# Kernel optimization log

Hardware: AMD Instinct MI355X
Metric: run time of the kernel (lower is better)

## Reference

```python
import jax, jax.numpy as jnp
import numpy as np

NUM_USERS = 100000
NUM_ITEMS = 50000
D = 64            # args.recdim
N_LAYERS = 3      # args.layer
NNZ = 4800000     # edges in the normalized bipartite adjacency (COO)
N = NUM_USERS + NUM_ITEMS


def setup_inputs() -> dict:
    key = jax.random.key(0)
    k1, k2, k3, k4, k5 = jax.random.split(key, 5)
    # LightGCN inits embeddings with normal(std=0.1)
    user_emb = 0.1 * jax.random.normal(k1, (NUM_USERS, D), dtype=jnp.float32)
    item_emb = 0.1 * jax.random.normal(k2, (NUM_ITEMS, D), dtype=jnp.float32)
    adj_rows = jax.random.randint(k3, (NNZ,), 0, N)
    adj_cols = jax.random.randint(k4, (NNZ,), 0, N)
    # stand-in for D^{-1/2} A D^{-1/2} normalized values
    adj_vals = jax.random.uniform(k5, (NNZ,), dtype=jnp.float32)
    return {"user_emb": user_emb, "item_emb": item_emb,
            "adj_vals": adj_vals, "adj_rows": adj_rows, "adj_cols": adj_cols}


def _spmm(rows, cols, vals, x, n):
    # sparse [n,n] @ dense [n,d] via gather + segment-sum (COO SpMM)
    return jax.ops.segment_sum(vals[:, None] * x[cols], rows, num_segments=n)


def reference(user_emb, item_emb, adj_vals, adj_rows, adj_cols):
    n_users = user_emb.shape[0]
    n = n_users + item_emb.shape[0]
    all_emb = jnp.concatenate([user_emb, item_emb], axis=0)  # [N, D]
    embs = [all_emb]
    for _ in range(N_LAYERS):  # fixed small hop count
        all_emb = _spmm(adj_rows, adj_cols, adj_vals, all_emb, n)
        embs.append(all_emb)
    light_out = jnp.mean(jnp.stack(embs, axis=1), axis=1)  # [N, D]
    users = light_out[:n_users]
    items = light_out[n_users:]
    return users, items
```

## Files before the change

kernel.cpp:

```cpp
#include <hip/hip_runtime.h>


#define NUSERS 100000
#define NITEMS 50000
#define NTOT   150000
#define DIM    64
#define NNZ_E  4800000

#define RPB     512
#define RSH     9
#define NBUCK   ((NTOT + RPB - 1) / RPB)
#define CHUNK_E 8192
#define NPART   ((NNZ_E + CHUNK_E - 1) / CHUNK_E)

__device__ __forceinline__ unsigned short benc(float f) {
    union { float f; unsigned u; } t; t.f = f;
    unsigned r = t.u + 0x7FFFu + ((t.u >> 16) & 1u);
    return (unsigned short)(r >> 16);
}
__device__ __forceinline__ float blo(unsigned g) { return __uint_as_float(g << 16); }
__device__ __forceinline__ float bhi(unsigned g) { return __uint_as_float(g & 0xFFFF0000u); }

__global__ void __launch_bounds__(512)
partA1_kernel(const int* __restrict__ rows, int* __restrict__ cntmatT) {
    __shared__ int l[NBUCK];
    int p = blockIdx.x;
    int c0 = p * CHUNK_E;
    int c1 = c0 + CHUNK_E; if (c1 > NNZ_E) c1 = NNZ_E;
    for (int k = threadIdx.x; k < NBUCK; k += 512) l[k] = 0;
    __syncthreads();
    for (int e = c0 + threadIdx.x; e < c1; e += 512)
        atomicAdd(&l[rows[e] >> RSH], 1);
    __syncthreads();
    for (int k = threadIdx.x; k < NBUCK; k += 512)
        cntmatT[(size_t)k * NPART + p] = l[k];
}

__global__ void __launch_bounds__(1024)
colscan1_kernel(const int* __restrict__ cntmatT, int* __restrict__ runoffT,
                int* __restrict__ colTotal) {
    __shared__ int t[1024];
    int b = blockIdx.x;
    int tid = threadIdx.x;
    int v = (tid < NPART) ? cntmatT[(size_t)b * NPART + tid] : 0;
    t[tid] = v;
    __syncthreads();
    for (int ofs = 1; ofs < 1024; ofs <<= 1) {
        int a = (tid >= ofs) ? t[tid - ofs] : 0;
        __syncthreads();
        t[tid] += a;
        __syncthreads();
    }
    if (tid < NPART) runoffT[(size_t)b * NPART + tid] = t[tid] - v;
    if (tid == NPART - 1) colTotal[b] = t[tid];
}

__global__ void colscan2_kernel(const int* __restrict__ colTotal, int* __restrict__ bptr) {
    __shared__ int t[512];
    int tid = threadIdx.x;
    int v = (tid < NBUCK) ? colTotal[tid] : 0;
    t[tid] = v;
    __syncthreads();
    for (int ofs = 1; ofs < 512; ofs <<= 1) {
        int a = (tid >= ofs) ? t[tid - ofs] : 0;
        __syncthreads();
        t[tid] += a;
        __syncthreads();
    }
    if (tid < NBUCK) bptr[tid] = t[tid] - v;
    if (tid == 511) bptr[NBUCK] = t[511];
}

__global__ void __launch_bounds__(512)
partA2_kernel(const int* __restrict__ rows, const int* __restrict__ cols,
              const float* __restrict__ vals, const int* __restrict__ runoffT,
              const int* __restrict__ bptr, int2* __restrict__ tmp) {
    __shared__ int cur[NBUCK];
    int p = blockIdx.x;
    int c0 = p * CHUNK_E;
    int c1 = c0 + CHUNK_E; if (c1 > NNZ_E) c1 = NNZ_E;
    for (int k = threadIdx.x; k < NBUCK; k += 512)
        cur[k] = bptr[k] + runoffT[(size_t)k * NPART + p];
    __syncthreads();
    for (int e = c0 + threadIdx.x; e < c1; e += 512) {
        int r = rows[e];
        int b = r >> RSH, rl = r & (RPB - 1);
        int q = atomicAdd(&cur[b], 1);
        tmp[q] = make_int2(cols[e] | (rl << 18), __float_as_int(vals[e]));
    }
}

__global__ void __launch_bounds__(1024)
partB_kernel(const int* __restrict__ bptr, const int2* __restrict__ tmp,
             unsigned* __restrict__ fin, int* __restrict__ rowptr) {
    __shared__ int cnt[RPB];
    __shared__ int cur[RPB];
    int b = blockIdx.x;
    int bb0 = bptr[b], bb1 = bptr[b + 1];
    int tid = threadIdx.x;
    if (tid < RPB) cnt[tid] = 0;
    __syncthreads();
    for (int e = bb0 + tid; e < bb1; e += 1024)
        atomicAdd(&cnt[((unsigned)tmp[e].x) >> 18], 1);
    __syncthreads();
    int v = 0;
    if (tid < RPB) { v = cnt[tid]; cur[tid] = v; }
    __syncthreads();
    for (int ofs = 1; ofs < RPB; ofs <<= 1) {
        int a = (tid < RPB && tid >= ofs) ? cur[tid - ofs] : 0;
        __syncthreads();
        if (tid < RPB) cur[tid] += a;
        __syncthreads();
    }
    if (tid < RPB) {
        int excl = cur[tid] - v;
        int row = b * RPB + tid;
        if (row < NTOT) rowptr[row] = bb0 + excl;
        cur[tid] = excl;
    }
    if (b == NBUCK - 1 && tid == 0) rowptr[NTOT] = bb1;
    __syncthreads();
    for (int e = bb0 + tid; e < bb1; e += 1024) {
        int2 t = tmp[e];
        int rl = ((unsigned)t.x) >> 18;
        int q = bb0 + atomicAdd(&cur[rl], 1);
        float val = __int_as_float(t.y);
        unsigned qq = (unsigned)__float2int_rn(val * 16384.f);
        if (qq > 16383u) qq = 16383u;
        fin[q] = (((unsigned)t.x & 0x3FFFFu) << 14) | qq;
    }
}

__global__ void convert_kernel(const float2* __restrict__ user, const float2* __restrict__ item,
                               unsigned* __restrict__ xh2) {
    int i = blockIdx.x * blockDim.x + threadIdx.x;
    if (i >= NTOT * 32) return;
    float2 v = (i < NUSERS * 32) ? user[i] : item[i - NUSERS * 32];
    xh2[i] = (unsigned)benc(v.x) | ((unsigned)benc(v.y) << 16);
}

__global__ void __launch_bounds__(256)
spmm_kernel(const int* __restrict__ rowptr, const unsigned* __restrict__ ed,
            const uint4* __restrict__ xin, uint4* __restrict__ yout,
            const float4* __restrict__ user, const float4* __restrict__ item,
            const uint4* __restrict__ y1, float4* __restrict__ out, int last) {
    int wid = blockIdx.x * (blockDim.x >> 6) + (threadIdx.x >> 6);
    int lane = threadIdx.x & 63;
    int oct = lane >> 3, s = lane & 7;
    int r = wid * 8 + oct;
    if (r >= NTOT) return;
    int start = rowptr[r];
    int end   = rowptr[r + 1];
    const float SCL = 1.f / 16384.f;
    float a0 = 0.f, a1 = 0.f, a2 = 0.f, a3 = 0.f, a4 = 0.f, a5 = 0.f, a6 = 0.f, a7 = 0.f;
    int i = start;
    for (; i + 8 <= end; i += 8) {
        unsigned e[8];
#pragma unroll
        for (int u = 0; u < 8; ++u) e[u] = ed[i + u];
        uint4 g[8];
#pragma unroll
        for (int u = 0; u < 8; ++u) g[u] = xin[(size_t)(e[u] >> 14) * 8 + s];
#pragma unroll
        for (int u = 0; u < 8; ++u) {
            float v = (float)(e[u] & 0x3FFFu) * SCL;
            a0 += v * blo(g[u].x); a1 += v * bhi(g[u].x);
            a2 += v * blo(g[u].y); a3 += v * bhi(g[u].y);
            a4 += v * blo(g[u].z); a5 += v * bhi(g[u].z);
            a6 += v * blo(g[u].w); a7 += v * bhi(g[u].w);
        }
    }
    for (; i < end; ++i) {
        unsigned e = ed[i];
        uint4 g = xin[(size_t)(e >> 14) * 8 + s];
        float v = (float)(e & 0x3FFFu) * SCL;
        a0 += v * blo(g.x); a1 += v * bhi(g.x);
        a2 += v * blo(g.y); a3 += v * bhi(g.y);
        a4 += v * blo(g.z); a5 += v * bhi(g.z);
        a6 += v * blo(g.w); a7 += v * bhi(g.w);
    }
    if (!last) {
        uint4 o;
        o.x = (unsigned)benc(a0) | ((unsigned)benc(a1) << 16);
        o.y = (unsigned)benc(a2) | ((unsigned)benc(a3) << 16);
        o.z = (unsigned)benc(a4) | ((unsigned)benc(a5) << 16);
        o.w = (unsigned)benc(a6) | ((unsigned)benc(a7) << 16);
        yout[(size_t)r * 8 + s] = o;
    } else {
        size_t f4 = (size_t)r * 16 + 2 * s;
        float4 x0a = (r < NUSERS) ? user[f4]     : item[f4     - (size_t)NUSERS * 16];
        float4 x0b = (r < NUSERS) ? user[f4 + 1] : item[f4 + 1 - (size_t)NUSERS * 16];
        uint4 u1 = y1[(size_t)r * 8 + s];
        uint4 u2 = xin[(size_t)r * 8 + s];
        float4 oa, ob;
        oa.x = 0.25f * (x0a.x + blo(u1.x) + blo(u2.x) + a0);
        oa.y = 0.25f * (x0a.y + bhi(u1.x) + bhi(u2.x) + a1);
        oa.z = 0.25f * (x0a.z + blo(u1.y) + blo(u2.y) + a2);
        oa.w = 0.25f * (x0a.w + bhi(u1.y) + bhi(u2.y) + a3);
        ob.x = 0.25f * (x0b.x + blo(u1.z) + blo(u2.z) + a4);
        ob.y = 0.25f * (x0b.y + bhi(u1.z) + bhi(u2.z) + a5);
        ob.z = 0.25f * (x0b.z + blo(u1.w) + blo(u2.w) + a6);
        ob.w = 0.25f * (x0b.w + bhi(u1.w) + bhi(u2.w) + a7);
        out[f4]     = oa;
        out[f4 + 1] = ob;
    }
}

extern "C" void kernel_launch(void* const* d_in, const int* in_sizes, int n_in,
                              void* d_out, int out_size, void* d_ws, size_t ws_size,
                              hipStream_t stream) {
    const float* user = (const float*)d_in[0];
    const float* item = (const float*)d_in[1];
    const float* vals = (const float*)d_in[2];
    const int*   rows = (const int*)d_in[3];
    const int*   cols = (const int*)d_in[4];
    float* out = (float*)d_out;

    char* w = (char*)d_ws;
    int2*     tmp      = (int2*)w;     w += (size_t)NNZ_E * 8;
    unsigned* fin      = (unsigned*)w; w += (size_t)NNZ_E * 4;
    unsigned* bufA     = (unsigned*)w; w += (size_t)NTOT * DIM * 2;
    unsigned* bufB     = (unsigned*)w; w += (size_t)NTOT * DIM * 2;
    int*      rowptr   = (int*)w;      w += (size_t)(NTOT + 1) * 4;
    int*      cntmatT  = (int*)w;      w += (size_t)NPART * NBUCK * 4;
    int*      runoffT  = (int*)w;      w += (size_t)NPART * NBUCK * 4;
    int*      colTotal = (int*)w;      w += (size_t)NBUCK * 4;
    int*      bptr     = (int*)w;

    const int blk = 256;
    const int gConv = (NTOT * 32 + blk - 1) / blk;
    const int gSpmm = (NTOT / 8 + 3) / 4;

    partA1_kernel<<<NPART, 512, 0, stream>>>(rows, cntmatT);
    colscan1_kernel<<<NBUCK, 1024, 0, stream>>>(cntmatT, runoffT, colTotal);
    colscan2_kernel<<<1, 512, 0, stream>>>(colTotal, bptr);
    partA2_kernel<<<NPART, 512, 0, stream>>>(rows, cols, vals, runoffT, bptr, tmp);
    partB_kernel<<<NBUCK, 1024, 0, stream>>>(bptr, tmp, fin, rowptr);

    convert_kernel<<<gConv, blk, 0, stream>>>((const float2*)user, (const float2*)item, bufA);

    spmm_kernel<<<gSpmm, blk, 0, stream>>>(rowptr, fin, (const uint4*)bufA, (uint4*)bufB,
                                           (const float4*)user, (const float4*)item,
                                           (const uint4*)bufB, (float4*)out, 0);
    spmm_kernel<<<gSpmm, blk, 0, stream>>>(rowptr, fin, (const uint4*)bufB, (uint4*)bufA,
                                           (const float4*)user, (const float4*)item,
                                           (const uint4*)bufB, (float4*)out, 0);
    spmm_kernel<<<gSpmm, blk, 0, stream>>>(rowptr, fin, (const uint4*)bufA, (uint4*)bufA,
                                           (const float4*)user, (const float4*)item,
                                           (const uint4*)bufB, (float4*)out, 1);
}
```

Baseline: 531.2 us.

## Fuse edge partition passes with local chunk sort and column-binned row ordering

Replaces the separate count and scatter passes with a single per-chunk kernel that sorts each chunk by bucket in shared memory and writes it contiguously. The second pass gathers each bucket's segments through a binary search over chunk offsets. Within each row it also orders edges by column block to improve locality of the SpMM gathers. Buckets shrink to 256 rows, and edge values are now quantized to 12 bits instead of 14 to make room for the column index. This trades accuracy and extra per-edge search work for fewer global scatter passes and better cache behavior in the three SpMM layers.

```diff
diff --git a/kernel.cpp b/kernel.cpp
--- a/kernel.cpp
+++ b/kernel.cpp
@@ -7,11 +7,14 @@
 #define DIM    64
 #define NNZ_E  4800000
 
-#define RPB     512
-#define RSH     9
-#define NBUCK   ((NTOT + RPB - 1) / RPB)
+#define RPB     256
+#define RSH     8
+#define NBUCK   586
 #define CHUNK_E 8192
 #define NPART   ((NNZ_E + CHUNK_E - 1) / CHUNK_E)
+#define NCB     37
+#define CSH     12
+#define NBIN    (RPB * NCB)
 
 __device__ __forceinline__ unsigned short benc(float f) {
     union { float f; unsigned u; } t; t.f = f;
@@ -22,27 +25,73 @@
 __device__ __forceinline__ float bhi(unsigned g) { return __uint_as_float(g & 0xFFFF0000u); }
 
 __global__ void __launch_bounds__(512)
-partA1_kernel(const int* __restrict__ rows, int* __restrict__ cntmatT) {
-    __shared__ int l[NBUCK];
+partA2_kernel(const int* __restrict__ rows, const int* __restrict__ cols,
+              const float* __restrict__ vals, int* __restrict__ cntmat,
+              int* __restrict__ segoff, int2* __restrict__ tmp) {
+    __shared__ int2 buf[CHUNK_E];
+    __shared__ int cnt[NBUCK];
+    __shared__ int st[512];
     int p = blockIdx.x;
     int c0 = p * CHUNK_E;
     int c1 = c0 + CHUNK_E; if (c1 > NNZ_E) c1 = NNZ_E;
-    for (int k = threadIdx.x; k < NBUCK; k += 512) l[k] = 0;
-    __syncthreads();
-    for (int e = c0 + threadIdx.x; e < c1; e += 512)
-        atomicAdd(&l[rows[e] >> RSH], 1);
-    __syncthreads();
-    for (int k = threadIdx.x; k < NBUCK; k += 512)
-        cntmatT[(size_t)k * NPART + p] = l[k];
+    int nb = c1 - c0;
+    int tid = threadIdx.x;
+    for (int k = tid; k < NBUCK; k += 512) cnt[k] = 0;
+    __syncthreads();
+    int rloc[16];
+#pragma unroll
+    for (int u = 0; u < 16; ++u) {
+        int e = c0 + tid + u * 512;
+        rloc[u] = (e < c1) ? rows[e] : -1;
+        if (rloc[u] >= 0) atomicAdd(&cnt[rloc[u] >> RSH], 1);
+    }
+    __syncthreads();
+    int t0 = tid * 2;
+    int cA = (t0     < NBUCK) ? cnt[t0]     : 0;
+    int cB = (t0 + 1 < NBUCK) ? cnt[t0 + 1] : 0;
+    int s = cA + cB;
+    st[tid] = s;
+    __syncthreads();
+    for (int ofs = 1; ofs < 512; ofs <<= 1) {
+        int a = (tid >= ofs) ? st[tid - ofs] : 0;
+        __syncthreads();
+        st[tid] += a;
+        __syncthreads();
+    }
+    int P = st[tid] - s;
+    if (t0 < NBUCK) {
+        cnt[t0] = P;
+        segoff[(size_t)p * NBUCK + t0] = P;
+        cntmat[(size_t)p * NBUCK + t0] = cA;
+    }
+    if (t0 + 1 < NBUCK) {
+        cnt[t0 + 1] = P + cA;
+        segoff[(size_t)p * NBUCK + t0 + 1] = P + cA;
+        cntmat[(size_t)p * NBUCK + t0 + 1] = cB;
+    }
+    __syncthreads();
+#pragma unroll
+    for (int u = 0; u < 16; ++u) {
+        int e = c0 + tid + u * 512;
+        if (rloc[u] >= 0) {
+            int r = rloc[u];
+            int b = r >> RSH, rl = r & (RPB - 1);
+            int q = atomicAdd(&cnt[b], 1);
+            buf[q] = make_int2(cols[e] | (rl << 18), __float_as_int(vals[e]));
+        }
+    }
+    __syncthreads();
+    for (int k = tid; k < nb; k += 512)
+        tmp[c0 + k] = buf[k];
 }
 
 __global__ void __launch_bounds__(1024)
-colscan1_kernel(const int* __restrict__ cntmatT, int* __restrict__ runoffT,
+colscan1_kernel(const int* __restrict__ cntmat, int* __restrict__ runoffT,
                 int* __restrict__ colTotal) {
     __shared__ int t[1024];
     int b = blockIdx.x;
     int tid = threadIdx.x;
-    int v = (tid < NPART) ? cntmatT[(size_t)b * NPART + tid] : 0;
+    int v = (tid < NPART) ? cntmat[(size_t)tid * NBUCK + b] : 0;
     t[tid] = v;
     __syncthreads();
     for (int ofs = 1; ofs < 1024; ofs <<= 1) {
@@ -51,83 +100,96 @@
         t[tid] += a;
         __syncthreads();
     }
-    if (tid < NPART) runoffT[(size_t)b * NPART + tid] = t[tid] - v;
-    if (tid == NPART - 1) colTotal[b] = t[tid];
-}
-
-__global__ void colscan2_kernel(const int* __restrict__ colTotal, int* __restrict__ bptr) {
-    __shared__ int t[512];
+    if (tid < NPART) runoffT[(size_t)b * (NPART + 1) + tid] = t[tid] - v;
+    if (tid == NPART - 1) {
+        runoffT[(size_t)b * (NPART + 1) + NPART] = t[tid];
+        colTotal[b] = t[tid];
+    }
+}
+
+__global__ void __launch_bounds__(1024)
+colscan2_kernel(const int* __restrict__ colTotal, int* __restrict__ bptr) {
+    __shared__ int t[1024];
     int tid = threadIdx.x;
     int v = (tid < NBUCK) ? colTotal[tid] : 0;
     t[tid] = v;
     __syncthreads();
-    for (int ofs = 1; ofs < 512; ofs <<= 1) {
+    for (int ofs = 1; ofs < 1024; ofs <<= 1) {
         int a = (tid >= ofs) ? t[tid - ofs] : 0;
         __syncthreads();
         t[tid] += a;
         __syncthreads();
     }
     if (tid < NBUCK) bptr[tid] = t[tid] - v;
-    if (tid == 511) bptr[NBUCK] = t[511];
-}
-
-__global__ void __launch_bounds__(512)
-partA2_kernel(const int* __restrict__ rows, const int* __restrict__ cols,
-              const float* __restrict__ vals, const int* __restrict__ runoffT,
-              const int* __restrict__ bptr, int2* __restrict__ tmp) {
-    __shared__ int cur[NBUCK];
-    int p = blockIdx.x;
-    int c0 = p * CHUNK_E;
-    int c1 = c0 + CHUNK_E; if (c1 > NNZ_E) c1 = NNZ_E;
-    for (int k = threadIdx.x; k < NBUCK; k += 512)
-        cur[k] = bptr[k] + runoffT[(size_t)k * NPART + p];
-    __syncthreads();
-    for (int e = c0 + threadIdx.x; e < c1; e += 512) {
-        int r = rows[e];
-        int b = r >> RSH, rl = r & (RPB - 1);
-        int q = atomicAdd(&cur[b], 1);
-        tmp[q] = make_int2(cols[e] | (rl << 18), __float_as_int(vals[e]));
-    }
+    if (tid == 1023) bptr[NBUCK] = t[1023];
 }
 
 __global__ void __launch_bounds__(1024)
-partB_kernel(const int* __restrict__ bptr, const int2* __restrict__ tmp,
-             unsigned* __restrict__ fin, int* __restrict__ rowptr) {
-    __shared__ int cnt[RPB];
-    __shared__ int cur[RPB];
+partBF_kernel(const int* __restrict__ bptr, const int* __restrict__ runoffT,
+              const int* __restrict__ segoff, const int2* __restrict__ tmp,
+              unsigned* __restrict__ fin, int* __restrict__ rowptr) {
+    __shared__ int cnt[NBIN];
+    __shared__ int st[1024];
+    __shared__ int runoff[NPART + 1];
+    __shared__ int soff[NPART];
     int b = blockIdx.x;
-    int bb0 = bptr[b], bb1 = bptr[b + 1];
+    int bb0 = bptr[b];
     int tid = threadIdx.x;
-    if (tid < RPB) cnt[tid] = 0;
-    __syncthreads();
-    for (int e = bb0 + tid; e < bb1; e += 1024)
-        atomicAdd(&cnt[((unsigned)tmp[e].x) >> 18], 1);
-    __syncthreads();
-    int v = 0;
-    if (tid < RPB) { v = cnt[tid]; cur[tid] = v; }
-    __syncthreads();
-    for (int ofs = 1; ofs < RPB; ofs <<= 1) {
-        int a = (tid < RPB && tid >= ofs) ? cur[tid - ofs] : 0;
-        __syncthreads();
-        if (tid < RPB) cur[tid] += a;
-        __syncthreads();
-    }
+    for (int k = tid; k < NBIN; k += 1024) cnt[k] = 0;
+    if (tid <= NPART) runoff[tid] = runoffT[(size_t)b * (NPART + 1) + tid];
+    if (tid < NPART)  soff[tid]   = segoff[(size_t)tid * NBUCK + b];
+    __syncthreads();
+    int nb = runoff[NPART];
+    for (int j = tid; j < nb; j += 1024) {
+        int lo = 0, hi = NPART;
+        while (hi - lo > 1) { int mid = (lo + hi) >> 1; if (runoff[mid] <= j) lo = mid; else hi = mid; }
+        int src = lo * CHUNK_E + soff[lo] + (j - runoff[lo]);
+        int x = tmp[src].x;
+        int key = ((x >> 18) & 255) * NCB + ((x & 0x3FFFF) >> CSH);
+        atomicAdd(&cnt[key], 1);
+    }
+    __syncthreads();
+    int t0 = tid * 10;
+    int c[10];
+    int s = 0;
+#pragma unroll
+    for (int u = 0; u < 10; ++u) {
+        int idx = t0 + u;
+        c[u] = (idx < NBIN) ? cnt[idx] : 0;
+        s += c[u];
+    }
+    st[tid] = s;
+    __syncthreads();
+    for (int ofs = 1; ofs < 1024; ofs <<= 1) {
+        int a = (tid >= ofs) ? st[tid - ofs] : 0;
+        __syncthreads();
+        st[tid] += a;
+        __syncthreads();
+    }
+    int P = st[tid] - s;
+#pragma unroll
+    for (int u = 0; u < 10; ++u) {
+        int idx = t0 + u;
+        if (idx < NBIN) { cnt[idx] = P; P += c[u]; }
+    }
+    __syncthreads();
     if (tid < RPB) {
-        int excl = cur[tid] - v;
-        int row = b * RPB + tid;
-        if (row < NTOT) rowptr[row] = bb0 + excl;
-        cur[tid] = excl;
-    }
-    if (b == NBUCK - 1 && tid == 0) rowptr[NTOT] = bb1;
-    __syncthreads();
-    for (int e = bb0 + tid; e < bb1; e += 1024) {
-        int2 t = tmp[e];
-        int rl = ((unsigned)t.x) >> 18;
-        int q = bb0 + atomicAdd(&cur[rl], 1);
-        float val = __int_as_float(t.y);
-        unsigned qq = (unsigned)__float2int_rn(val * 16384.f);
-        if (qq > 16383u) qq = 16383u;
-        fin[q] = (((unsigned)t.x & 0x3FFFFu) << 14) | qq;
+        int r = b * RPB + tid;
+        if (r < NTOT) rowptr[r] = bb0 + cnt[tid * NCB];
+    }
+    if (b == NBUCK - 1 && tid == 0) rowptr[NTOT] = bb0 + nb;
+    __syncthreads();
+    for (int j = tid; j < nb; j += 1024) {
+        int lo = 0, hi = NPART;
+        while (hi - lo > 1) { int mid = (lo + hi) >> 1; if (runoff[mid] <= j) lo = mid; else hi = mid; }
+        int src = lo * CHUNK_E + soff[lo] + (j - runoff[lo]);
+        int2 t = tmp[src];
+        int x = t.x;
+        int key = ((x >> 18) & 255) * NCB + ((x & 0x3FFFF) >> CSH);
+        int q = atomicAdd(&cnt[key], 1);
+        unsigned qq = (unsigned)__float2int_rn(__int_as_float(t.y) * 4096.f);
+        if (qq > 4095u) qq = 4095u;
+        fin[bb0 + q] = ((unsigned)x & 0x3FFFFu) | (qq << 20);
     }
 }
 
@@ -151,7 +213,7 @@
     if (r >= NTOT) return;
     int start = rowptr[r];
     int end   = rowptr[r + 1];
-    const float SCL = 1.f / 16384.f;
+    const float SCL = 1.f / 4096.f;
     float a0 = 0.f, a1 = 0.f, a2 = 0.f, a3 = 0.f, a4 = 0.f, a5 = 0.f, a6 = 0.f, a7 = 0.f;
     int i = start;
     for (; i + 8 <= end; i += 8) {
@@ -160,10 +222,10 @@
         for (int u = 0; u < 8; ++u) e[u] = ed[i + u];
         uint4 g[8];
 #pragma unroll
-        for (int u = 0; u < 8; ++u) g[u] = xin[(size_t)(e[u] >> 14) * 8 + s];
+        for (int u = 0; u < 8; ++u) g[u] = xin[(size_t)(e[u] & 0x3FFFFu) * 8 + s];
 #pragma unroll
         for (int u = 0; u < 8; ++u) {
-            float v = (float)(e[u] & 0x3FFFu) * SCL;
+            float v = (float)(e[u] >> 20) * SCL;
             a0 += v * blo(g[u].x); a1 += v * bhi(g[u].x);
             a2 += v * blo(g[u].y); a3 += v * bhi(g[u].y);
             a4 += v * blo(g[u].z); a5 += v * bhi(g[u].z);
@@ -172,8 +234,8 @@
     }
     for (; i < end; ++i) {
         unsigned e = ed[i];
-        uint4 g = xin[(size_t)(e >> 14) * 8 + s];
-        float v = (float)(e & 0x3FFFu) * SCL;
+        uint4 g = xin[(size_t)(e & 0x3FFFFu) * 8 + s];
+        float v = (float)(e >> 20) * SCL;
         a0 += v * blo(g.x); a1 += v * bhi(g.x);
         a2 += v * blo(g.y); a3 += v * bhi(g.y);
         a4 += v * blo(g.z); a5 += v * bhi(g.z);
@@ -221,9 +283,10 @@
     unsigned* fin      = (unsigned*)w; w += (size_t)NNZ_E * 4;
     unsigned* bufA     = (unsigned*)w; w += (size_t)NTOT * DIM * 2;
     unsigned* bufB     = (unsigned*)w; w += (size_t)NTOT * DIM * 2;
+    int*      cntmat   = (int*)w;      w += (size_t)NPART * NBUCK * 4;
+    int*      runoffT  = (int*)w;      w += (size_t)NBUCK * (NPART + 1) * 4;
+    int*      segoff   = (int*)w;      w += (size_t)NPART * NBUCK * 4;
     int*      rowptr   = (int*)w;      w += (size_t)(NTOT + 1) * 4;
-    int*      cntmatT  = (int*)w;      w += (size_t)NPART * NBUCK * 4;
-    int*      runoffT  = (int*)w;      w += (size_t)NPART * NBUCK * 4;
     int*      colTotal = (int*)w;      w += (size_t)NBUCK * 4;
     int*      bptr     = (int*)w;
 
@@ -231,11 +294,10 @@
     const int gConv = (NTOT * 32 + blk - 1) / blk;
     const int gSpmm = (NTOT / 8 + 3) / 4;
 
-    partA1_kernel<<<NPART, 512, 0, stream>>>(rows, cntmatT);
-    colscan1_kernel<<<NBUCK, 1024, 0, stream>>>(cntmatT, runoffT, colTotal);
-    colscan2_kernel<<<1, 512, 0, stream>>>(colTotal, bptr);
-    partA2_kernel<<<NPART, 512, 0, stream>>>(rows, cols, vals, runoffT, bptr, tmp);
-    partB_kernel<<<NBUCK, 1024, 0, stream>>>(bptr, tmp, fin, rowptr);
+    partA2_kernel<<<NPART, 512, 0, stream>>>(rows, cols, vals, cntmat, segoff, tmp);
+    colscan1_kernel<<<NBUCK, 1024, 0, stream>>>(cntmat, runoffT, colTotal);
+    colscan2_kernel<<<1, 1024, 0, stream>>>(colTotal, bptr);
+    partBF_kernel<<<NBUCK, 1024, 0, stream>>>(bptr, runoffT, segoff, tmp, fin, rowptr);
 
     convert_kernel<<<gConv, blk, 0, stream>>>((const float2*)user, (const float2*)item, bufA);
 
```

Measured after the change: 489.3 us. 7.9% less time.
